# Performance work log

Hardware: AMD Instinct MI355X
Metric: run time of the kernel (lower is better)

The kernel has to match this reference:

```python
import jax, jax.numpy as jnp
import numpy as np

NUM_HEADS = 8

def _proj(x, w, b):
    # 1x1x1 Conv3d == pointwise linear over channel dim
    return jnp.einsum('bcxyz,oc->boxyz', x, w) + b[None, :, None, None, None]


def setup_inputs() -> dict:
    key = jax.random.key(0)
    ks = jax.random.split(key, 9)
    B, C, X, Y, Z = 2, 256, 48, 48, 48
    s = 0.05
    return {
        'x':  jax.random.normal(ks[0], (B, C, X, Y, Z), dtype=jnp.float32),
        'wq': jax.random.normal(ks[1], (C, C), dtype=jnp.float32) * s,
        'bq': jax.random.normal(ks[2], (C,), dtype=jnp.float32) * s,
        'wk': jax.random.normal(ks[3], (C, C), dtype=jnp.float32) * s,
        'bk': jax.random.normal(ks[4], (C,), dtype=jnp.float32) * s,
        'wv': jax.random.normal(ks[5], (C, C), dtype=jnp.float32) * s,
        'bv': jax.random.normal(ks[6], (C,), dtype=jnp.float32) * s,
        'wo': jax.random.normal(ks[7], (C, C), dtype=jnp.float32) * s,
        'bo': jax.random.normal(ks[8], (C,), dtype=jnp.float32) * s,
    }


def reference(x, wq, bq, wk, bk, wv, bv, wo, bo):
    B, C, X, Y, Z = x.shape
    H = NUM_HEADS
    P = C // H  # per-head channels
    q = _proj(x, wq, bq).reshape(B, H, P, X, Y, Z)
    k = _proj(x, wk, bk).reshape(B, H, P, X, Y, Z)
    v = _proj(x, wv, bv).reshape(B, H, P, X, Y, Z)
    # torch einsum 'bnxyzc,bmxyzc->bnmxy' contracts z and per-head channel c
    scores = jnp.einsum('bncxyz,bmcxyz->bnmxy', q, k) / jnp.sqrt(jnp.float32(P))
    # torch F.softmax(dim=-1) on [b,n,m,x,y] -> softmax over y axis (faithful)
    attn = jax.nn.softmax(scores, axis=-1)
    # torch 'bnmxy,bmxyzc->bnxyzc', then permute/reshape back to [B,C,X,Y,Z]
    out = jnp.einsum('bnmxy,bmcxyz->bncxyz', attn, v).reshape(B, C, X, Y, Z)
    return _proj(out, wo, bo)
```

## Files before the change

kernel.cpp:

```cpp
#include <hip/hip_runtime.h>
#include <hip/hip_bf16.h>
#include <stdint.h>


#define S_TOT 110592
#define NBX   2304

typedef unsigned short u16;
typedef __attribute__((ext_vector_type(8))) short bf16x8;
typedef __attribute__((ext_vector_type(4))) float f32x4;

__device__ __forceinline__ u16 f2b(float f){
  union { float f; uint32_t u; } v; v.f = f;
  uint32_t u = v.u;
  return (u16)((u + 0x7fffu + ((u >> 16) & 1u)) >> 16);
}
__device__ __forceinline__ float b2f(u16 h){
  union { float f; uint32_t u; } v; v.u = ((uint32_t)h) << 16; return v.f;
}
__device__ __forceinline__ f32x4 mfma16(bf16x8 a, bf16x8 b, f32x4 c){
  return __builtin_amdgcn_mfma_f32_16x16x32_bf16(a, b, c, 0, 0, 0);
}

__global__ __launch_bounds__(256) void k_prep(
    const float* __restrict__ wq, const float* __restrict__ wk,
    const float* __restrict__ wv, const float* __restrict__ wo,
    u16* __restrict__ img)
{
  int idx = blockIdx.x * 256 + threadIdx.x;
  if (idx < 131072){
    int ck = idx >> 14, rem = idx & 16383;
    int r = rem >> 5, i = rem & 31;
    int c = ck * 32 + i;
    float v = (r < 256) ? wq[r * 256 + c] : wk[(r - 256) * 256 + c];
    img[idx] = f2b(v);
  } else if (idx < 196608){
    int l = idx - 131072;
    int ck = l >> 13, rem = l & 8191;
    int r = rem >> 5, i = rem & 31;
    img[idx] = f2b(wv[r * 256 + ck * 32 + i]);
  } else if (idx < 262144){
    int l = idx - 196608;
    int ck = l >> 13, rem = l & 8191;
    int r = rem >> 5, i = rem & 31;
    img[idx] = f2b(wo[r * 256 + ck * 32 + i]);
  }
}

#define K1_LDS 151552
__global__ __launch_bounds__(1024, 4) void k_qk_scores(
    const float* __restrict__ x, const u16* __restrict__ wimg,
    const float* __restrict__ bq, const float* __restrict__ bk,
    float* __restrict__ scores)
{
  extern __shared__ char lds[];
  u16* xT  = (u16*)lds;
  u16* qkz = (u16*)(lds + 49152);
  float* ps = (float*)(lds + 147456);

  const int tid  = threadIdx.x;
  const int wave = tid >> 6, lane = tid & 63;
  const int l15 = lane & 15, l4 = lane >> 4;
  const int bx = blockIdx.x, b = blockIdx.y;
  const int s0 = bx * 96;
  const float* xb = x + (size_t)b * 256 * S_TOT;

  #pragma unroll
  for (int it = 0; it < 3; it++){
    int e = it * 1024 + tid;
    int z = e % 96, c16 = e / 96;
    const float* px = xb + (size_t)(c16 * 8) * S_TOT + s0 + z;
    union { uint4 q; u16 h[8]; } u;
    #pragma unroll
    for (int i = 0; i < 8; i++) u.h[i] = f2b(px[(size_t)i * S_TOT]);
    *(uint4*)((char*)xT + z * 512 + ((c16 ^ (z & 7)) << 4)) = u.q;
  }
  __syncthreads();

  const int proj = wave >> 3;
  const int rb = (wave & 7) * 32;
  const float* bias = proj ? bk : bq;

  f32x4 acc[2][6];
  #pragma unroll
  for (int fr = 0; fr < 2; fr++){
    f32x4 iv;
    #pragma unroll
    for (int j = 0; j < 4; j++) iv[j] = bias[rb + fr * 16 + l4 * 4 + j];
    #pragma unroll
    for (int fc = 0; fc < 6; fc++) acc[fr][fc] = iv;
  }
  #pragma unroll
  for (int ck = 0; ck < 8; ck++){
    bf16x8 af[2], bfr[6];
    #pragma unroll
    for (int fr = 0; fr < 2; fr++){
      int row = wave * 32 + fr * 16 + l15;
      af[fr] = *(const bf16x8*)(wimg + ck * 16384 + row * 32 + l4 * 8);
    }
    #pragma unroll
    for (int fc = 0; fc < 6; fc++){
      int z = fc * 16 + l15;
      bfr[fc] = *(const bf16x8*)((char*)xT + z * 512 + (((ck * 4 + l4) ^ (l15 & 7)) << 4));
    }
    #pragma unroll
    for (int fr = 0; fr < 2; fr++)
      #pragma unroll
      for (int fc = 0; fc < 6; fc++)
        acc[fr][fc] = mfma16(af[fr], bfr[fc], acc[fr][fc]);
  }

  #pragma unroll
  for (int fr = 0; fr < 2; fr++){
    int och = proj * 256 + rb + fr * 16 + l4 * 4;
    #pragma unroll
    for (int fc = 0; fc < 6; fc++){
      int z = fc * 16 + l15;
      ushort4 u;
      u.x = f2b(acc[fr][fc][0]); u.y = f2b(acc[fr][fc][1]);
      u.z = f2b(acc[fr][fc][2]); u.w = f2b(acc[fr][fc][3]);
      *(ushort4*)((char*)qkz + z * 1024 + ((((och >> 3) ^ z) & 63) << 4)
                  + (och & 7) * 2) = u;
    }
  }
  __syncthreads();

  {
    const int ca = l15 * 32 + l4 * 8;
    const int cb = 256 + (l15 & 7) * 32 + l4 * 8;
    const int zb = (wave >> 3) * 48 + (wave & 7) * 6;
    f32x4 sc = {0.f, 0.f, 0.f, 0.f};
    #pragma unroll
    for (int zi = 0; zi < 6; zi++){
      int zl = zb + zi;
      bf16x8 aq  = *(const bf16x8*)((char*)qkz + zl * 1024 + ((((ca >> 3) ^ zl) & 63) << 4));
      bf16x8 bk8 = *(const bf16x8*)((char*)qkz + zl * 1024 + ((((cb >> 3) ^ zl) & 63) << 4));
      sc = mfma16(aq, bk8, sc);
    }
    if (l4 < 2 && l15 < 8){
      #pragma unroll
      for (int j = 0; j < 4; j++)
        ps[wave * 64 + (l4 * 4 + j) * 8 + l15] = sc[j];
    }
  }
  __syncthreads();

  if (tid < 128){
    int h = tid >> 6, idx = tid & 63;
    float s = 0.f;
    #pragma unroll
    for (int w = 0; w < 8; w++) s += ps[(h * 8 + w) * 64 + idx];
    scores[(size_t)(b * 64 + idx) * NBX + bx * 2 + h] = s * 0.17677669529663687f;
  }
}

__global__ __launch_bounds__(256) void k_softmax(
    const float* __restrict__ scores, float* __restrict__ attn)
{
  int row  = blockIdx.x * 4 + (threadIdx.x >> 6);
  int lane = threadIdx.x & 63;
  const float* src = scores + (size_t)row * 48;
  float v = (lane < 48) ? src[lane] : -1e30f;
  float m = v;
  #pragma unroll
  for (int off = 32; off; off >>= 1) m = fmaxf(m, __shfl_xor(m, off));
  float e = (lane < 48) ? __expf(v - m) : 0.f;
  float s = e;
  #pragma unroll
  for (int off = 32; off; off >>= 1) s += __shfl_xor(s, off);
  if (lane < 48) attn[(size_t)row * 48 + lane] = e / s;
}

#define K3_LDS 49664
__global__ __launch_bounds__(512, 4) void k_out(
    const float* __restrict__ x, const u16* __restrict__ wvimg,
    const u16* __restrict__ woimg, const float* __restrict__ bv,
    const float* __restrict__ bo, const float* __restrict__ attn,
    float* __restrict__ out)
{
  extern __shared__ char lds[];
  u16* xT = (u16*)lds;
  u16* vl = (u16*)lds;
  u16* oT = (u16*)lds;
  float* atl = (float*)(lds + 49152);

  const int tid  = threadIdx.x;
  const int wave = tid >> 6, lane = tid & 63;
  const int l15 = lane & 15, l4 = lane >> 4;
  const int bx = blockIdx.x, b = blockIdx.y;
  const int s0 = bx * 96;
  const float* xb = x + (size_t)b * 256 * S_TOT;

  if (tid < 128)
    atl[tid] = attn[(size_t)(b * 64 + (tid & 63)) * NBX + bx * 2 + (tid >> 6)];

  #pragma unroll
  for (int it = 0; it < 6; it++){
    int e = it * 512 + tid;
    int z = e % 96, c16 = e / 96;
    const float* px = xb + (size_t)(c16 * 8) * S_TOT + s0 + z;
    union { uint4 q; u16 h[8]; } u;
    #pragma unroll
    for (int i = 0; i < 8; i++) u.h[i] = f2b(px[(size_t)i * S_TOT]);
    *(uint4*)((char*)xT + z * 512 + ((c16 ^ (z & 7)) << 4)) = u.q;
  }
  __syncthreads();

  f32x4 vac[2][6];
  #pragma unroll
  for (int fr = 0; fr < 2; fr++){
    f32x4 iv;
    #pragma unroll
    for (int j = 0; j < 4; j++) iv[j] = bv[wave * 32 + fr * 16 + l4 * 4 + j];
    #pragma unroll
    for (int fc = 0; fc < 6; fc++) vac[fr][fc] = iv;
  }
  #pragma unroll
  for (int ck = 0; ck < 8; ck++){
    bf16x8 af[2], bfr[6];
    #pragma unroll
    for (int fr = 0; fr < 2; fr++){
      int row = wave * 32 + fr * 16 + l15;
      af[fr] = *(const bf16x8*)(wvimg + ck * 8192 + row * 32 + l4 * 8);
    }
    #pragma unroll
    for (int fc = 0; fc < 6; fc++){
      int z = fc * 16 + l15;
      bfr[fc] = *(const bf16x8*)((char*)xT + z * 512 + (((ck * 4 + l4) ^ (l15 & 7)) << 4));
    }
    #pragma unroll
    for (int fr = 0; fr < 2; fr++)
      #pragma unroll
      for (int fc = 0; fc < 6; fc++)
        vac[fr][fc] = mfma16(af[fr], bfr[fc], vac[fr][fc]);
  }
  __syncthreads();

  #pragma unroll
  for (int fr = 0; fr < 2; fr++){
    int o0 = wave * 32 + fr * 16 + l4 * 4;
    #pragma unroll
    for (int fc = 0; fc < 6; fc++){
      int z = fc * 16 + l15;
      ushort4 u;
      u.x = f2b(vac[fr][fc][0]); u.y = f2b(vac[fr][fc][1]);
      u.z = f2b(vac[fr][fc][2]); u.w = f2b(vac[fr][fc][3]);
      *(ushort4*)((char*)vl + z * 512 + (((o0 >> 3) ^ (z & 7)) << 4) + (o0 & 7) * 2) = u;
    }
  }
  __syncthreads();

  #pragma unroll
  for (int it = 0; it < 6; it++){
    int e = it * 512 + tid;
    int c16 = e & 31, z = e >> 5;
    int r = c16 & 3, hn = c16 >> 2;
    const float* at = atl + ((z >= 48) ? 64 : 0);
    float a[8] = {0,0,0,0,0,0,0,0};
    #pragma unroll
    for (int m = 0; m < 8; m++){
      union { uint4 q; u16 h[8]; } v8;
      v8.q = *(const uint4*)((char*)vl + z * 512 + (((m * 4 + r) ^ (z & 7)) << 4));
      float am = at[hn * 8 + m];
      #pragma unroll
      for (int i = 0; i < 8; i++) a[i] = fmaf(am, b2f(v8.h[i]), a[i]);
    }
    union { uint4 q; u16 h[8]; } pk;
    #pragma unroll
    for (int i = 0; i < 8; i++) pk.h[i] = f2b(a[i]);
    __syncthreads();
    *(uint4*)((char*)oT + z * 512 + ((c16 ^ (z & 7)) << 4)) = pk.q;
  }
  __syncthreads();

  f32x4 oac[2][6];
  #pragma unroll
  for (int fr = 0; fr < 2; fr++){
    f32x4 iv;
    #pragma unroll
    for (int j = 0; j < 4; j++) iv[j] = bo[wave * 32 + fr * 16 + l4 * 4 + j];
    #pragma unroll
    for (int fc = 0; fc < 6; fc++) oac[fr][fc] = iv;
  }
  #pragma unroll
  for (int ck = 0; ck < 8; ck++){
    bf16x8 af[2], bfr[6];
    #pragma unroll
    for (int fr = 0; fr < 2; fr++){
      int row = wave * 32 + fr * 16 + l15;
      af[fr] = *(const bf16x8*)(woimg + ck * 8192 + row * 32 + l4 * 8);
    }
    #pragma unroll
    for (int fc = 0; fc < 6; fc++){
      int z = fc * 16 + l15;
      bfr[fc] = *(const bf16x8*)((char*)oT + z * 512 + (((ck * 4 + l4) ^ (l15 & 7)) << 4));
    }
    #pragma unroll
    for (int fr = 0; fr < 2; fr++)
      #pragma unroll
      for (int fc = 0; fc < 6; fc++)
        oac[fr][fc] = mfma16(af[fr], bfr[fc], oac[fr][fc]);
  }

  #pragma unroll
  for (int fr = 0; fr < 2; fr++)
    #pragma unroll
    for (int fc = 0; fc < 6; fc++)
      #pragma unroll
      for (int j = 0; j < 4; j++){
        int o = wave * 32 + fr * 16 + l4 * 4 + j;
        int z = fc * 16 + l15;
        out[(size_t)(b * 256 + o) * S_TOT + s0 + z] = oac[fr][fc][j];
      }
}

extern "C" void kernel_launch(void* const* d_in, const int* in_sizes, int n_in,
                              void* d_out, int out_size, void* d_ws, size_t ws_size,
                              hipStream_t stream) {
  (void)in_sizes; (void)n_in; (void)out_size; (void)ws_size;
  const float* x  = (const float*)d_in[0];
  const float* wq = (const float*)d_in[1];
  const float* bq = (const float*)d_in[2];
  const float* wk = (const float*)d_in[3];
  const float* bk = (const float*)d_in[4];
  const float* wv = (const float*)d_in[5];
  const float* bv = (const float*)d_in[6];
  const float* wo = (const float*)d_in[7];
  const float* bo = (const float*)d_in[8];
  float* out = (float*)d_out;

  char* ws = (char*)d_ws;
  u16*  wimg   = (u16*)ws;
  u16*  wvimg  = wimg + 131072;
  u16*  woimg  = wimg + 196608;
  float* scores = (float*)(ws + 524288);
  float* attn   = (float*)(ws + 1703936);

  hipFuncSetAttribute((const void*)k_qk_scores,
                      hipFuncAttributeMaxDynamicSharedMemorySize, K1_LDS);

  k_prep<<<1024, 256, 0, stream>>>(wq, wk, wv, wo, wimg);
  k_qk_scores<<<dim3(1152, 2), 1024, K1_LDS, stream>>>(x, wimg, bq, bk, scores);
  k_softmax<<<1536, 256, 0, stream>>>(scores, attn);
  k_out<<<dim3(1152, 2), 512, K3_LDS, stream>>>(x, wvimg, woimg, bv, bo, attn, out);
}
```

Before: 238.2 us.

## Shrink QK-scores LDS by reusing x tile buffer and processing z halves

The projected Q/K tile is now written over the x-transpose buffer and handled in two halves of 48 z values, with separate partial-sum buffers for each half. This cuts dynamic shared memory from about 148 KB to 56 KB, so the opt-in attribute call is dropped and more than one 1024-thread block could fit per CU. In exchange it adds extra barriers and serialises the score reduction into two phases.

Measured after the change: 239.1 us. Within noise of the previous version (+0.4%).

```diff
diff --git a/kernel.cpp b/kernel.cpp
--- a/kernel.cpp
+++ b/kernel.cpp
@@ -47,7 +47,7 @@
   }
 }
 
-#define K1_LDS 151552
+#define K1_LDS 57344
 __global__ __launch_bounds__(1024, 4) void k_qk_scores(
     const float* __restrict__ x, const u16* __restrict__ wimg,
     const float* __restrict__ bq, const float* __restrict__ bk,
@@ -55,8 +55,9 @@
 {
   extern __shared__ char lds[];
   u16* xT  = (u16*)lds;
-  u16* qkz = (u16*)(lds + 49152);
-  float* ps = (float*)(lds + 147456);
+  u16* qkz = (u16*)lds;
+  float* ps0 = (float*)(lds + 49152);
+  float* ps1 = (float*)(lds + 53248);
 
   const int tid  = threadIdx.x;
   const int wave = tid >> 6, lane = tid & 63;
@@ -109,30 +110,31 @@
       for (int fc = 0; fc < 6; fc++)
         acc[fr][fc] = mfma16(af[fr], bfr[fc], acc[fr][fc]);
   }
-
-  #pragma unroll
-  for (int fr = 0; fr < 2; fr++){
-    int och = proj * 256 + rb + fr * 16 + l4 * 4;
-    #pragma unroll
-    for (int fc = 0; fc < 6; fc++){
-      int z = fc * 16 + l15;
+  __syncthreads();
+
+  const int och = proj * 256 + rb + l4 * 4;
+  const int ca = l15 * 32 + l4 * 8;
+  const int cb = 256 + (l15 & 7) * 32 + l4 * 8;
+
+  #pragma unroll
+  for (int fr = 0; fr < 2; fr++){
+    int oc = och + fr * 16;
+    #pragma unroll
+    for (int fc = 0; fc < 3; fc++){
+      int zl = fc * 16 + l15;
       ushort4 u;
       u.x = f2b(acc[fr][fc][0]); u.y = f2b(acc[fr][fc][1]);
       u.z = f2b(acc[fr][fc][2]); u.w = f2b(acc[fr][fc][3]);
-      *(ushort4*)((char*)qkz + z * 1024 + ((((och >> 3) ^ z) & 63) << 4)
-                  + (och & 7) * 2) = u;
-    }
-  }
-  __syncthreads();
-
+      *(ushort4*)((char*)qkz + zl * 1024 + ((((oc >> 3) ^ zl) & 63) << 4)
+                  + (oc & 7) * 2) = u;
+    }
+  }
+  __syncthreads();
   {
-    const int ca = l15 * 32 + l4 * 8;
-    const int cb = 256 + (l15 & 7) * 32 + l4 * 8;
-    const int zb = (wave >> 3) * 48 + (wave & 7) * 6;
     f32x4 sc = {0.f, 0.f, 0.f, 0.f};
     #pragma unroll
-    for (int zi = 0; zi < 6; zi++){
-      int zl = zb + zi;
+    for (int zi = 0; zi < 3; zi++){
+      int zl = wave * 3 + zi;
       bf16x8 aq  = *(const bf16x8*)((char*)qkz + zl * 1024 + ((((ca >> 3) ^ zl) & 63) << 4));
       bf16x8 bk8 = *(const bf16x8*)((char*)qkz + zl * 1024 + ((((cb >> 3) ^ zl) & 63) << 4));
       sc = mfma16(aq, bk8, sc);
@@ -140,17 +142,52 @@
     if (l4 < 2 && l15 < 8){
       #pragma unroll
       for (int j = 0; j < 4; j++)
-        ps[wave * 64 + (l4 * 4 + j) * 8 + l15] = sc[j];
-    }
-  }
-  __syncthreads();
-
-  if (tid < 128){
-    int h = tid >> 6, idx = tid & 63;
+        ps0[wave * 64 + (l4 * 4 + j) * 8 + l15] = sc[j];
+    }
+  }
+  __syncthreads();
+
+  if (tid < 64){
     float s = 0.f;
     #pragma unroll
-    for (int w = 0; w < 8; w++) s += ps[(h * 8 + w) * 64 + idx];
-    scores[(size_t)(b * 64 + idx) * NBX + bx * 2 + h] = s * 0.17677669529663687f;
+    for (int w = 0; w < 16; w++) s += ps0[w * 64 + tid];
+    scores[(size_t)(b * 64 + tid) * NBX + bx * 2] = s * 0.17677669529663687f;
+  }
+  #pragma unroll
+  for (int fr = 0; fr < 2; fr++){
+    int oc = och + fr * 16;
+    #pragma unroll
+    for (int fc = 3; fc < 6; fc++){
+      int zl = (fc - 3) * 16 + l15;
+      ushort4 u;
+      u.x = f2b(acc[fr][fc][0]); u.y = f2b(acc[fr][fc][1]);
+      u.z = f2b(acc[fr][fc][2]); u.w = f2b(acc[fr][fc][3]);
+      *(ushort4*)((char*)qkz + zl * 1024 + ((((oc >> 3) ^ zl) & 63) << 4)
+                  + (oc & 7) * 2) = u;
+    }
+  }
+  __syncthreads();
+  {
+    f32x4 sc = {0.f, 0.f, 0.f, 0.f};
+    #pragma unroll
+    for (int zi = 0; zi < 3; zi++){
+      int zl = wave * 3 + zi;
+      bf16x8 aq  = *(const bf16x8*)((char*)qkz + zl * 1024 + ((((ca >> 3) ^ zl) & 63) << 4));
+      bf16x8 bk8 = *(const bf16x8*)((char*)qkz + zl * 1024 + ((((cb >> 3) ^ zl) & 63) << 4));
+      sc = mfma16(aq, bk8, sc);
+    }
+    if (l4 < 2 && l15 < 8){
+      #pragma unroll
+      for (int j = 0; j < 4; j++)
+        ps1[wave * 64 + (l4 * 4 + j) * 8 + l15] = sc[j];
+    }
+  }
+  __syncthreads();
+  if (tid < 64){
+    float s = 0.f;
+    #pragma unroll
+    for (int w = 0; w < 16; w++) s += ps1[w * 64 + tid];
+    scores[(size_t)(b * 64 + tid) * NBX + bx * 2 + 1] = s * 0.17677669529663687f;
   }
 }
 
@@ -336,9 +373,6 @@
   float* scores = (float*)(ws + 524288);
   float* attn   = (float*)(ws + 1703936);
 
-  hipFuncSetAttribute((const void*)k_qk_scores,
-                      hipFuncAttributeMaxDynamicSharedMemorySize, K1_LDS);
-
   k_prep<<<1024, 256, 0, stream>>>(wq, wk, wv, wo, wimg);
   k_qk_scores<<<dim3(1152, 2), 1024, K1_LDS, stream>>>(x, wimg, bq, bk, scores);
   k_softmax<<<1536, 256, 0, stream>>>(scores, attn);
```
